# Performance work log

Hardware: AMD Instinct MI355X
Metric: run time of the kernel (lower is better)

## Reference

```python
import jax, jax.numpy as jnp
import numpy as np

B, C, L = 16, 512, 8192
R = 16  # reduction_ratio
H = C // R


def setup_inputs() -> dict:
    key = jax.random.key(0)
    k_x, k_w1, k_b1, k_w2, k_b2 = jax.random.split(key, 5)
    # PyTorch Linear default init: U(-1/sqrt(fan_in), 1/sqrt(fan_in))
    lim1 = 1.0 / np.sqrt(C)
    lim2 = 1.0 / np.sqrt(H)
    return {
        "x": jax.random.normal(k_x, (B, C, L), dtype=jnp.float32),
        "w1": jax.random.uniform(k_w1, (H, C), minval=-lim1, maxval=lim1, dtype=jnp.float32),
        "b1": jax.random.uniform(k_b1, (H,), minval=-lim1, maxval=lim1, dtype=jnp.float32),
        "w2": jax.random.uniform(k_w2, (C, H), minval=-lim2, maxval=lim2, dtype=jnp.float32),
        "b2": jax.random.uniform(k_b2, (C,), minval=-lim2, maxval=lim2, dtype=jnp.float32),
    }


def reference(x, w1, b1, w2, b2):
    # x: [B, C, L]
    s = jnp.mean(x, axis=2)                      # [B, C]  global avg pool
    h = jax.nn.relu(s @ w1.T + b1)               # [B, H]
    g = jax.nn.sigmoid(h @ w2.T + b2)            # [B, C]  channel gates
    return x * g[:, :, None]                     # [B, C, L]
```

## Files before the change

### kernel.cpp

```cpp
#include <hip/hip_runtime.h>
#include <math.h>

#define BB 16
#define CC 512
#define LL 8192
#define HH 32
#define BC (BB * CC)

typedef float fv4 __attribute__((ext_vector_type(4)));

__global__ __launch_bounds__(256) void k_mean(const float* __restrict__ x,
                                              float* __restrict__ s) {
    const int row = blockIdx.x;
    const int tid = threadIdx.x;
    const fv4* xr = (const fv4*)(x + (size_t)row * LL);

    float acc = 0.0f;
#pragma unroll
    for (int i = 0; i < LL / 4 / 256; ++i) {
        fv4 v = xr[i * 256 + tid];
        acc += (v.x + v.y) + (v.z + v.w);
    }
#pragma unroll
    for (int off = 32; off > 0; off >>= 1)
        acc += __shfl_down(acc, off, 64);

    __shared__ float part[4];
    const int lane = tid & 63, wv = tid >> 6;
    if (lane == 0) part[wv] = acc;
    __syncthreads();
    if (tid == 0) {
        float t = (part[0] + part[1]) + (part[2] + part[3]);
        s[row] = t * (1.0f / (float)LL);
    }
}

__global__ __launch_bounds__(256) void k_scale_fused(
        const float* __restrict__ x,  const float* __restrict__ s,
        const float* __restrict__ w1, const float* __restrict__ b1,
        const float* __restrict__ w2, const float* __restrict__ b2,
        float* __restrict__ out) {
    const int bid   = (int)gridDim.x - 1 - (int)blockIdx.x;
    const int b     = bid >> 7;
    const int chunk = bid & 127;
    const int tid   = threadIdx.x;

    __shared__ float partial[HH][9];
    __shared__ float h[HH];
    __shared__ float g4[4];

    {
        const int j   = tid >> 3;
        const int seg = tid & 7;
        const float* srow = s  + b * CC + seg * 64;
        const float* wrow = w1 + (size_t)j * CC + seg * 64;
        float p = 0.0f;
#pragma unroll
        for (int c = 0; c < 64; ++c) p += srow[c] * wrow[c];
        partial[j][seg] = p;
    }
    __syncthreads();
    if (tid < HH) {
        float t = b1[tid];
#pragma unroll
        for (int k = 0; k < 8; ++k) t += partial[tid][k];
        h[tid] = t > 0.0f ? t : 0.0f;
    }
    __syncthreads();
    if (tid < 4) {
        const int c = chunk * 4 + tid;
        const float* wrow = w2 + (size_t)c * HH;
        float z = b2[c];
#pragma unroll
        for (int j = 0; j < HH; ++j) z += h[j] * wrow[j];
        g4[tid] = 1.0f / (1.0f + expf(-z));
    }
    __syncthreads();

#pragma unroll
    for (int r = 0; r < 4; ++r) {
        const int c = chunk * 4 + r;
        const size_t off = ((size_t)b * CC + c) * (size_t)LL;
        const fv4* xr  = (const fv4*)(x + off);
        fv4*       orr = (fv4*)(out + off);
        const float gate = g4[r];
#pragma unroll
        for (int i = 0; i < LL / 4 / 256; ++i) {
            fv4 v = xr[i * 256 + tid];
            v *= gate;
            __builtin_nontemporal_store(v, &orr[i * 256 + tid]);
        }
    }
}

extern "C" void kernel_launch(void* const* d_in, const int* in_sizes, int n_in,
                              void* d_out, int out_size, void* d_ws, size_t ws_size,
                              hipStream_t stream) {
    const float* x  = (const float*)d_in[0];
    const float* w1 = (const float*)d_in[1];
    const float* b1 = (const float*)d_in[2];
    const float* w2 = (const float*)d_in[3];
    const float* b2 = (const float*)d_in[4];
    float* out = (float*)d_out;

    float* s = (float*)d_ws;

    k_mean       <<<BC,   256, 0, stream>>>(x, s);
    k_scale_fused<<<BC/4, 256, 0, stream>>>(x, s, w1, b1, w2, b2, out);
}
```

Measured before the change: 127.5 us.

## Split batch in halves and overlap scaling of first half with second-half mean

The two-kernel pipeline becomes three launches. The first computes means for the first half of the batch-channel rows (launched in reverse order). The middle kernel scales the first half while computing means for the second half in the same grid. The last kernel scales the second half in reverse order, which is meant to reuse cache-resident data and reduce the idle tail between phases, at the cost of an extra launch.

```diff
diff --git a/kernel.cpp b/kernel.cpp
--- a/kernel.cpp
+++ b/kernel.cpp
@@ -6,49 +6,35 @@
 #define LL 8192
 #define HH 32
 #define BC (BB * CC)
+#define HALF (BC / 2)
 
 typedef float fv4 __attribute__((ext_vector_type(4)));
 
-__global__ __launch_bounds__(256) void k_mean(const float* __restrict__ x,
-                                              float* __restrict__ s) {
-    const int row = blockIdx.x;
-    const int tid = threadIdx.x;
+__device__ __forceinline__ void dev_mean_row(const float* __restrict__ x,
+                                             float* __restrict__ s,
+                                             int row, int tid, float* red) {
     const fv4* xr = (const fv4*)(x + (size_t)row * LL);
-
     float acc = 0.0f;
 #pragma unroll
-    for (int i = 0; i < LL / 4 / 256; ++i) {
+    for (int i = 0; i < 8; ++i) {
         fv4 v = xr[i * 256 + tid];
         acc += (v.x + v.y) + (v.z + v.w);
     }
 #pragma unroll
     for (int off = 32; off > 0; off >>= 1)
         acc += __shfl_down(acc, off, 64);
-
-    __shared__ float part[4];
-    const int lane = tid & 63, wv = tid >> 6;
-    if (lane == 0) part[wv] = acc;
+    if ((tid & 63) == 0) red[tid >> 6] = acc;
     __syncthreads();
-    if (tid == 0) {
-        float t = (part[0] + part[1]) + (part[2] + part[3]);
-        s[row] = t * (1.0f / (float)LL);
-    }
+    if (tid == 0)
+        s[row] = ((red[0] + red[1]) + (red[2] + red[3])) * (1.0f / (float)LL);
 }
 
-__global__ __launch_bounds__(256) void k_scale_fused(
+__device__ __forceinline__ void dev_scale4(
         const float* __restrict__ x,  const float* __restrict__ s,
         const float* __restrict__ w1, const float* __restrict__ b1,
         const float* __restrict__ w2, const float* __restrict__ b2,
-        float* __restrict__ out) {
-    const int bid   = (int)gridDim.x - 1 - (int)blockIdx.x;
-    const int b     = bid >> 7;
-    const int chunk = bid & 127;
-    const int tid   = threadIdx.x;
-
-    __shared__ float partial[HH][9];
-    __shared__ float h[HH];
-    __shared__ float g4[4];
-
+        float* __restrict__ out, int b, int c0, int tid,
+        float (*partial)[9], float* h, float* g4) {
     {
         const int j   = tid >> 3;
         const int seg = tid & 7;
@@ -63,12 +49,12 @@
     if (tid < HH) {
         float t = b1[tid];
 #pragma unroll
-        for (int k = 0; k < 8; ++k) t += partial[tid][k];
+        for (int q = 0; q < 8; ++q) t += partial[tid][q];
         h[tid] = t > 0.0f ? t : 0.0f;
     }
     __syncthreads();
     if (tid < 4) {
-        const int c = chunk * 4 + tid;
+        const int c = c0 + tid;
         const float* wrow = w2 + (size_t)c * HH;
         float z = b2[c];
 #pragma unroll
@@ -79,18 +65,61 @@
 
 #pragma unroll
     for (int r = 0; r < 4; ++r) {
-        const int c = chunk * 4 + r;
+        const int c = c0 + r;
         const size_t off = ((size_t)b * CC + c) * (size_t)LL;
         const fv4* xr  = (const fv4*)(x + off);
         fv4*       orr = (fv4*)(out + off);
         const float gate = g4[r];
 #pragma unroll
-        for (int i = 0; i < LL / 4 / 256; ++i) {
+        for (int i = 0; i < 8; ++i) {
             fv4 v = xr[i * 256 + tid];
             v *= gate;
             __builtin_nontemporal_store(v, &orr[i * 256 + tid]);
         }
     }
+}
+
+__global__ __launch_bounds__(256) void k_mean_c0(const float* __restrict__ x,
+                                                 float* __restrict__ s) {
+    __shared__ float red[4];
+    const int row = (int)gridDim.x - 1 - (int)blockIdx.x;
+    dev_mean_row(x, s, row, threadIdx.x, red);
+}
+
+__global__ __launch_bounds__(256) void k_scale0_mean1(
+        const float* __restrict__ x,  float* __restrict__ s,
+        const float* __restrict__ w1, const float* __restrict__ b1,
+        const float* __restrict__ w2, const float* __restrict__ b2,
+        float* __restrict__ out) {
+    __shared__ float red[4];
+    __shared__ float partial[HH][9];
+    __shared__ float h[HH];
+    __shared__ float g4[4];
+    const int tid = threadIdx.x;
+
+    if (blockIdx.x < HALF / 4) {
+        const int j  = blockIdx.x;
+        const int r0 = 4 * j;
+        dev_scale4(x, s, w1, b1, w2, b2, out, r0 >> 9, r0 & (CC - 1), tid,
+                   partial, h, g4);
+    } else {
+        const int row = HALF + ((int)blockIdx.x - HALF / 4);
+        dev_mean_row(x, s, row, tid, red);
+    }
+}
+
+__global__ __launch_bounds__(256) void k_scale_c1(
+        const float* __restrict__ x,  const float* __restrict__ s,
+        const float* __restrict__ w1, const float* __restrict__ b1,
+        const float* __restrict__ w2, const float* __restrict__ b2,
+        float* __restrict__ out) {
+    __shared__ float partial[HH][9];
+    __shared__ float h[HH];
+    __shared__ float g4[4];
+    const int j  = (int)gridDim.x - 1 - (int)blockIdx.x;
+    const int r0 = HALF + 4 * j;
+    dev_scale4(x, s, w1, b1, w2, b2, out, r0 >> 9, r0 & (CC - 1),
+               threadIdx.x, partial, h, g4);
 }
 
 extern "C" void kernel_launch(void* const* d_in, const int* in_sizes, int n_in,
@@ -105,6 +134,7 @@
 
     float* s = (float*)d_ws;
 
-    k_mean       <<<BC,   256, 0, stream>>>(x, s);
-    k_scale_fused<<<BC/4, 256, 0, stream>>>(x, s, w1, b1, w2, b2, out);
+    k_mean_c0     <<<HALF,            256, 0, stream>>>(x, s);
+    k_scale0_mean1<<<HALF / 4 + HALF, 256, 0, stream>>>(x, s, w1, b1, w2, b2, out);
+    k_scale_c1    <<<HALF / 4,        256, 0, stream>>>(x, s, w1, b1, w2, b2, out);
 }
```

New measurement: 139.2 us. 9.2% more time.
